# Performance work log

Measured on AMD Instinct MI355X. Metric: run time of the kernel, lower is better.

The kernel has to match this reference:

```python
import jax, jax.numpy as jnp
import numpy as np

B, NH, T, H, W = 2, 4, 8, 14, 14
DIM = 384
HD = DIM // NH  # 96 = head_dim = depthwise conv channels
N = T * H * W  # 1568 tokens, no cls
EPS = 1e-6


def _dwconv3d(x, w):
    # x: [BN, C, T, H, W], w: [C, 1, 3, 3, 3]; depthwise conv, stride 1, pad 1
    return jax.lax.conv_general_dilated(
        x, w, window_strides=(1, 1, 1), padding=[(1, 1)] * 3,
        feature_group_count=x.shape[1],
        dimension_numbers=('NCDHW', 'OIDHW', 'NCDHW'))


def _layernorm(x, g, b):
    m = jnp.mean(x, axis=-1, keepdims=True)
    v = jnp.var(x, axis=-1, keepdims=True)
    return (x - m) * jax.lax.rsqrt(v + EPS) * g + b


def _attention_pool(x4, conv_w, ln_g, ln_b, t, h, w):
    # x4: [B, nh, L, c] with L = t*h*w (no cls token)
    Bq, n, L, c = x4.shape
    y = x4.reshape(Bq * n, t, h, w, c).transpose(0, 4, 1, 2, 3)  # [(b nh), c, t, h, w]
    y = _dwconv3d(y, conv_w)
    y = y.transpose(0, 2, 3, 4, 1).reshape(Bq, n, L, c)
    return _layernorm(y, ln_g, ln_b)


def setup_inputs() -> dict:
    key = jax.random.key(0)
    ks = jax.random.split(key, 12)
    inp = {
        'x': jax.random.normal(ks[0], (B, N, DIM), jnp.float32),
        'qkv_w': jax.random.normal(ks[1], (3 * DIM, DIM), jnp.float32) * 0.02,
        'proj_w': jax.random.normal(ks[2], (DIM, DIM), jnp.float32) * 0.02,
        'proj_b': jnp.zeros((DIM,), jnp.float32),
        'pool_q_w': jax.random.normal(ks[3], (HD, 1, 3, 3, 3), jnp.float32) * 0.1,
        'pool_k_w': jax.random.normal(ks[4], (HD, 1, 3, 3, 3), jnp.float32) * 0.1,
        'pool_v_w': jax.random.normal(ks[5], (HD, 1, 3, 3, 3), jnp.float32) * 0.1,
        'norm_q_w': jnp.ones((HD,), jnp.float32), 'norm_q_b': jnp.zeros((HD,), jnp.float32),
        'norm_k_w': jnp.ones((HD,), jnp.float32), 'norm_k_b': jnp.zeros((HD,), jnp.float32),
        'norm_v_w': jnp.ones((HD,), jnp.float32), 'norm_v_b': jnp.zeros((HD,), jnp.float32),
        'rel_pos_h': jax.random.normal(ks[6], (2 * H - 1, HD), jnp.float32) * 0.02,
        'rel_pos_w': jax.random.normal(ks[7], (2 * W - 1, HD), jnp.float32) * 0.02,
        'rel_pos_t': jax.random.normal(ks[8], (2 * T - 1, HD), jnp.float32) * 0.02,
        't': T, 'h': H, 'w': W,
    }
    return inp


def reference(x, qkv_w, proj_w, proj_b, pool_q_w, pool_k_w, pool_v_w,
              norm_q_w, norm_q_b, norm_k_w, norm_k_b, norm_v_w, norm_v_b,
              rel_pos_h, rel_pos_w, rel_pos_t, t, h, w):
    Bq, Nq, _ = x.shape
    # fused QKV projection (qkv_bias=False)
    qkv = (x @ qkv_w.T).reshape(Bq, Nq, 3, NH, HD).transpose(2, 0, 3, 1, 4)
    q, k, v = qkv[0], qkv[1], qkv[2]  # [B, nh, N, hd]
    # pooled Q/K/V: depthwise conv3d + LayerNorm (stride 1 -> shapes preserved)
    q = _attention_pool(q, pool_q_w, norm_q_w, norm_q_b, t, h, w)
    k = _attention_pool(k, pool_k_w, norm_k_w, norm_k_b, t, h, w)
    v = _attention_pool(v, pool_v_w, norm_v_w, norm_v_b, t, h, w)

    scale = HD ** -0.5
    attn = jnp.einsum('bnqc,bnkc->bnqk', q * scale, k)  # [B, nh, N, N]

    # decomposed relative position biases (q_shape == k_shape, ratios == 1)
    dist_h = jnp.arange(h)[:, None] - jnp.arange(h)[None, :] + (h - 1)
    dist_w = jnp.arange(w)[:, None] - jnp.arange(w)[None, :] + (w - 1)
    dist_t = jnp.arange(t)[:, None] - jnp.arange(t)[None, :] + (t - 1)
    Rh = rel_pos_h[dist_h]  # [h, h, c]
    Rw = rel_pos_w[dist_w]  # [w, w, c]
    Rt = rel_pos_t[dist_t]  # [t, t, c]

    r_q = q.reshape(Bq, NH, t, h, w, HD)
    rel_h = jnp.einsum('bnthwc,hkc->bnthwk', r_q, Rh)  # [B,nh,t,h,w,kh]
    rel_w = jnp.einsum('bnthwc,wkc->bnthwk', r_q, Rw)  # [B,nh,t,h,w,kw]
    rel_t = jnp.einsum('bnthwc,tkc->bnthwk', r_q, Rt)  # [B,nh,t,h,w,kt]

    attn8 = attn.reshape(Bq, NH, t, h, w, t, h, w)
    attn8 = (attn8
             + rel_h[:, :, :, :, :, None, :, None]
             + rel_w[:, :, :, :, :, None, None, :]
             + rel_t[:, :, :, :, :, :, None, None])
    attn = jax.nn.softmax(attn8.reshape(Bq, NH, Nq, Nq), axis=-1)

    out = jnp.einsum('bnqk,bnkc->bnqc', attn, v)
    out = out + q  # residual pooling
    out = out.transpose(0, 2, 1, 3).reshape(Bq, Nq, DIM)
    out = out @ proj_w.T + proj_b
    return out
```

## Files before the change

kernel.cpp:

```cpp
#include <hip/hip_runtime.h>

#define B_    2
#define NH_   4
#define T_    8
#define H_    14
#define W_    14
#define HW_   196
#define HD_   96
#define DIM_  384
#define N_    1568
#define BH_   (B_*NH_)
#define BN_   (B_*N_)
#define BHN_  (BH_*N_)
#define CAUG_ 160

typedef unsigned short bf_t;
typedef unsigned int   u32;
typedef __attribute__((ext_vector_type(8))) short bf16x8;
typedef __attribute__((ext_vector_type(4))) float f32x4;

#define LOG2E 1.4426950408889634f
#define QSCALE_LOG2E 0.14724445f

static __device__ __forceinline__ float lo16(u32 v){ union{u32 i; float f;}x; x.i = v<<16;           return x.f; }
static __device__ __forceinline__ float hi16(u32 v){ union{u32 i; float f;}x; x.i = v & 0xffff0000u; return x.f; }
static __device__ __forceinline__ float b2f(bf_t v){ union{u32 i; float f;}x; x.i = ((u32)v)<<16;    return x.f; }
static __device__ __forceinline__ bf_t  f2b(float f){
  union{float f; u32 i;} x; x.f = f;
  return (bf_t)((x.i + 0x7fffu + ((x.i>>16)&1u)) >> 16);
}
static __device__ __forceinline__ u32 pack2(float a, float b){
  return (u32)f2b(a) | ((u32)f2b(b) << 16);
}

#define NA_ (BN_*DIM_)
#define NB_ (3*DIM_*DIM_)
#define NC_ (DIM_*DIM_)
#define CAST_BLOCKS ((NA_+NB_+NC_)/4/256)

__global__ __launch_bounds__(256) void k_cast(
    const float* __restrict__ a, bf_t* __restrict__ ad,
    const float* __restrict__ b, bf_t* __restrict__ bd,
    const float* __restrict__ c, bf_t* __restrict__ cd,
    const float* __restrict__ wq, const float* __restrict__ wk,
    const float* __restrict__ wv, float* __restrict__ tq,
    float* __restrict__ tk, float* __restrict__ tv){
  if (blockIdx.x < CAST_BLOCKS){
    const int i = blockIdx.x*256 + threadIdx.x;
    const int i4 = i*4;
    const float4* src; bf_t* dst; int off;
    if (i4 < NA_)           { src = (const float4*)a; dst = ad; off = i; }
    else if (i4 < NA_+NB_)  { src = (const float4*)b; dst = bd; off = i - NA_/4; }
    else                    { src = (const float4*)c; dst = cd; off = i - (NA_+NB_)/4; }
    const float4 v = src[off];
    ushort4 o; o.x = f2b(v.x); o.y = f2b(v.y); o.z = f2b(v.z); o.w = f2b(v.w);
    ((ushort4*)dst)[off] = o;
  } else {
    const int idx = (blockIdx.x - CAST_BLOCKS)*256 + threadIdx.x;
    if (idx >= 3*HD_*27) return;
    const int t = idx / (HD_*27), rem = idx % (HD_*27);
    const int ch = rem / 27, j = rem % 27;
    const float* s = (t==0)? wq : (t==1)? wk : wv;
    float* d       = (t==0)? tq : (t==1)? tk : tv;
    d[j*HD_ + ch] = s[ch*27 + j];
  }
}

__global__ __launch_bounds__(256) void k_qkv(const bf_t* __restrict__ Xb,
    const bf_t* __restrict__ Wb,
    bf_t* __restrict__ q, bf_t* __restrict__ k, bf_t* __restrict__ v){
  const int wid = threadIdx.x >> 6, lane = threadIdx.x & 63;
  const int wr = wid & 1, wc = wid >> 1;
  const int nl = lane & 15, quad = lane >> 4;
  const int r0 = blockIdx.x*64 + wr*32;
  const int c0 = blockIdx.y*128 + wc*64;
  f32x4 acc[2][4];
  #pragma unroll
  for (int i = 0; i < 2; ++i)
    #pragma unroll
    for (int j = 0; j < 4; ++j) acc[i][j] = (f32x4){0.f,0.f,0.f,0.f};
  const bf_t* A0 = Xb + (size_t)(r0 + nl)*DIM_ + quad*8;
  const bf_t* B0 = Wb + (size_t)(c0 + nl)*DIM_ + quad*8;
  #pragma unroll 2
  for (int k0 = 0; k0 < 12; ++k0){
    const bf16x8 a0 = *(const bf16x8*)(A0 + k0*32);
    const bf16x8 a1 = *(const bf16x8*)(A0 + 16*DIM_ + k0*32);
    bf16x8 bf[4];
    #pragma unroll
    for (int j = 0; j < 4; ++j) bf[j] = *(const bf16x8*)(B0 + (size_t)j*16*DIM_ + k0*32);
    #pragma unroll
    for (int j = 0; j < 4; ++j){
      acc[0][j] = __builtin_amdgcn_mfma_f32_16x16x32_bf16(a0, bf[j], acc[0][j], 0, 0, 0);
      acc[1][j] = __builtin_amdgcn_mfma_f32_16x16x32_bf16(a1, bf[j], acc[1][j], 0, 0, 0);
    }
  }
  #pragma unroll
  for (int i = 0; i < 2; ++i){
    #pragma unroll
    for (int r = 0; r < 4; ++r){
      const int m  = r0 + i*16 + quad*4 + r;
      const int bb = m / N_, nn = m % N_;
      #pragma unroll
      for (int j = 0; j < 4; ++j){
        const int col = c0 + j*16 + nl;
        const int s = col / DIM_, rem = col - s*DIM_;
        const int head = rem / HD_, hc = rem % HD_;
        bf_t* dst = (s==0) ? q : (s==1) ? k : v;
        dst[((size_t)(bb*NH_ + head)*N_ + nn)*HD_ + hc] = f2b(acc[i][j][r]);
      }
    }
  }
}

static __device__ __forceinline__ void conv_core(
    const bf_t* __restrict__ base, const float2* __restrict__ wgt,
    int n, int c0, float& v0, float& v1){
  const int tt = n / HW_; const int rm = n % HW_;
  const int hh = rm / W_, ww = rm % W_;
  u32 data[27];
  #pragma unroll
  for (int j = 0; j < 27; ++j){
    const int dt = j/9 - 1, dh = (j%9)/3 - 1, dw = j%3 - 1;
    const int t2 = tt+dt, h2 = hh+dh, w2 = ww+dw;
    const bool ok = ((unsigned)t2 < (unsigned)T_) && ((unsigned)h2 < (unsigned)H_)
                 && ((unsigned)w2 < (unsigned)W_);
    const int nn = ok ? (t2*HW_ + h2*W_ + w2) : n;
    const u32 d = *(const u32*)(base + (size_t)nn*HD_ + c0);
    data[j] = ok ? d : 0u;
  }
  v0 = 0.f; v1 = 0.f;
  #pragma unroll
  for (int j = 0; j < 27; ++j){
    v0 = fmaf(wgt[j].x, lo16(data[j]), v0);
    v1 = fmaf(wgt[j].y, hi16(data[j]), v1);
  }
}

static __device__ __forceinline__ void ln_butterfly(
    float v0, float v1, float& mean, float& rstd){
  float s  = v0 + v1;
  float s2 = v0*v0 + v1*v1;
  #pragma unroll
  for (int off = 32; off > 0; off >>= 1){
    s  += __shfl_xor(s,  off);
    s2 += __shfl_xor(s2, off);
  }
  mean = s * (1.f/HD_);
  const float var = fmaxf(s2*(1.f/HD_) - mean*mean, 0.f);
  rstd = rsqrtf(var + 1e-6f);
}

__global__ __launch_bounds__(256) void k_pool_all(
    const bf_t* __restrict__ qr_, const bf_t* __restrict__ kr_, const bf_t* __restrict__ vr_,
    const float* __restrict__ wtq, const float* __restrict__ wtk, const float* __restrict__ wtv,
    const float* __restrict__ gq, const float* __restrict__ bq,
    const float* __restrict__ gk, const float* __restrict__ bk,
    const float* __restrict__ gv, const float* __restrict__ bv,
    const float* __restrict__ rph, const float* __restrict__ rpw,
    const float* __restrict__ rpt,
    bf_t* __restrict__ qp, bf_t* __restrict__ Qaug,
    bf_t* __restrict__ Kt, bf_t* __restrict__ Vtt){
  __shared__ float qs[4][HD_];
  const int wid = threadIdx.x >> 6, lane = threadIdx.x & 63;
  const int bix = blockIdx.x;

  if (bix < BHN_/4){
    const int token = bix*4 + wid;
    const int bh = token / N_, n = token % N_;
    const int c0 = (lane < 48) ? 2*lane : 0;
    float2 wgt[27];
    #pragma unroll
    for (int j = 0; j < 27; ++j) wgt[j] = *(const float2*)(wtq + j*HD_ + c0);
    float v0, v1;
    conv_core(qr_ + (size_t)bh*N_*HD_, wgt, n, c0, v0, v1);
    if (lane >= 48){ v0 = 0.f; v1 = 0.f; }
    float mean, rstd;
    ln_butterfly(v0, v1, mean, rstd);
    if (lane < 48){
      const float y0 = (v0 - mean)*rstd*gq[c0]   + bq[c0];
      const float y1 = (v1 - mean)*rstd*gq[c0+1] + bq[c0+1];
      ((u32*)qp)  [(size_t)token*48 + lane] = pack2(y0, y1);
      ((u32*)Qaug)[(size_t)token*80 + lane] = pack2(y0*QSCALE_LOG2E, y1*QSCALE_LOG2E);
      qs[wid][c0] = y0; qs[wid][c0+1] = y1;
    }
    __syncthreads();
    const int tt = n / HW_; const int rm = n % HW_;
    const int hh = rm / W_, ww = rm % W_;
    if (lane < 36){
      const float* tb; int idx;
      if (lane < 14)      { tb = rph; idx = hh - lane      + 13; }
      else if (lane < 28) { tb = rpw; idx = ww - (lane-14) + 13; }
      else                { tb = rpt; idx = tt - (lane-28) +  7; }
      const float4* t4 = (const float4*)(tb + (size_t)idx*HD_);
      float acc = 0.f;
      #pragma unroll
      for (int i = 0; i < 24; ++i){
        const float4 rv = t4[i];
        acc += qs[wid][4*i]*rv.x + qs[wid][4*i+1]*rv.y
             + qs[wid][4*i+2]*rv.z + qs[wid][4*i+3]*rv.w;
      }
      Qaug[(size_t)token*CAUG_ + HD_ + lane] = f2b(acc * LOG2E);
    } else {
      Qaug[(size_t)token*CAUG_ + HD_ + lane] = 0;
    }
  } else if (bix < BHN_/2){
    const int token = (bix - BHN_/4)*4 + wid;
    const int bh = token / N_, n = token % N_;
    const int c0 = (lane < 48) ? 2*lane : 0;
    float2 wgt[27];
    #pragma unroll
    for (int j = 0; j < 27; ++j) wgt[j] = *(const float2*)(wtk + j*HD_ + c0);
    float v0, v1;
    conv_core(kr_ + (size_t)bh*N_*HD_, wgt, n, c0, v0, v1);
    if (lane >= 48){ v0 = 0.f; v1 = 0.f; }
    float mean, rstd;
    ln_butterfly(v0, v1, mean, rstd);
    const int tl = n >> 4, nr = n & 15;
    if (lane < 48){
      const float y0 = (v0 - mean)*rstd*gk[c0]   + bk[c0];
      const float y1 = (v1 - mean)*rstd*gk[c0+1] + bk[c0+1];
      const size_t idx = ((((size_t)bh*98 + tl)*5 + (lane>>4))*64
                         + ((lane&15)>>2)*16 + nr)*4 + (lane&3);
      ((u32*)Kt)[idx] = pack2(y0, y1);
    } else {
      const int tt = n / HW_; const int rm = n % HW_;
      const int hh = rm / W_, ww = rm % W_;
      const int m = lane - 48;
      u32 p[2];
      #pragma unroll
      for (int h2 = 0; h2 < 2; ++h2){
        u32 w_ = 0;
        #pragma unroll
        for (int e = 0; e < 2; ++e){
          const int jj = 4*m + 2*h2 + e;
          bool on = (jj < 14) ? (jj == hh) : (jj < 28) ? (jj-14 == ww)
                   : (jj < 36) ? (jj-28 == tt) : false;
          if (on) w_ |= (0x3F80u << (16*e));
        }
        p[h2] = w_;
      }
      const size_t base = ((((size_t)bh*98 + tl)*5 + (3 + (m>>3)))*64
                          + ((m&7)>>1)*16 + nr)*4 + 2*(m&1);
      *(uint2*)((u32*)Kt + base) = make_uint2(p[0], p[1]);
    }
  } else {
    const int tok0 = ((bix - BHN_/2)*4 + wid)*8;
    const int bh = tok0 / N_, n0 = tok0 % N_;
    const bf_t* base = vr_ + (size_t)bh*N_*HD_;
    const int c0 = (lane < 48) ? 2*lane : 0;
    float2 wgt[27];
    #pragma unroll
    for (int j = 0; j < 27; ++j) wgt[j] = *(const float2*)(wtv + j*HD_ + c0);
    const float gg0 = gv[c0], gg1 = gv[c0+1], bb0 = bv[c0], bb1 = bv[c0+1];
    u32 acc[8];
    #pragma unroll 1
    for (int t8 = 0; t8 < 8; ++t8){
      float v0, v1;
      conv_core(base, wgt, n0 + t8, c0, v0, v1);
      if (lane >= 48){ v0 = 0.f; v1 = 0.f; }
      float mean, rstd;
      ln_butterfly(v0, v1, mean, rstd);
      acc[t8] = pack2((v0 - mean)*rstd*gg0 + bb0, (v1 - mean)*rstd*gg1 + bb1);
    }
    if (lane < 48){
      u32 lo[4], hi[4];
      #pragma unroll
      for (int i = 0; i < 4; ++i){
        lo[i] = (acc[2*i] & 0xffffu)  | (acc[2*i+1] << 16);
        hi[i] = (acc[2*i] >> 16)      | (acc[2*i+1] & 0xffff0000u);
      }
      const int pr = n0 >> 5, qd = (n0 & 31) >> 3;
      const int ct0 = lane >> 3, nl0 = 2*(lane & 7);
      bf_t* g0 = Vtt + ((((size_t)bh*49 + pr)*6 + ct0)*64 + qd*16 + nl0)*8;
      *(uint4*)g0       = make_uint4(lo[0], lo[1], lo[2], lo[3]);
      *(uint4*)(g0 + 8) = make_uint4(hi[0], hi[1], hi[2], hi[3]);
    }
  }
}

__global__ __launch_bounds__(512) void k_attn(
    const bf_t* __restrict__ Qaug, const bf_t* __restrict__ Kt,
    const bf_t* __restrict__ Vtt, const bf_t* __restrict__ qp,
    bf_t* __restrict__ attb){
  __shared__ __align__(16) short Pb[8][16][40];
  __shared__ float Os[8][16][96];
  __shared__ float ms[8][16], ls[8][16];
  const int wid = threadIdx.x >> 6, lane = threadIdx.x & 63;
  const int bh = blockIdx.x / 98, qt = blockIdx.x % 98;
  const int q0 = qt*16;
  const int nl = lane & 15, quad = lane >> 4;

  bf16x8 qa[5];
  {
    const bf_t* Qrow = Qaug + ((size_t)bh*N_ + q0 + nl)*CAUG_ + quad*8;
    #pragma unroll
    for (int i = 0; i < 5; ++i) qa[i] = *(const bf16x8*)(Qrow + i*32);
  }
  short* Pw = &Pb[wid][0][0];

  f32x4 O[6];
  #pragma unroll
  for (int i = 0; i < 6; ++i) O[i] = (f32x4){0.f,0.f,0.f,0.f};
  float mc[4]   = {0.f,0.f,0.f,0.f};
  float rmax[4] = {-3e38f,-3e38f,-3e38f,-3e38f};
  float l[4]    = {0.f,0.f,0.f,0.f};

  auto s_tile = [&](int tl, int half){
    const bf_t* Kp = Kt + (((size_t)bh*98 + tl)*5*64 + lane)*8;
    f32x4 s = (f32x4){0.f,0.f,0.f,0.f};
    #pragma unroll
    for (int i = 0; i < 5; ++i)
      s = __builtin_amdgcn_mfma_f32_16x16x32_bf16(qa[i], *(const bf16x8*)(Kp + i*512), s, 0, 0, 0);
    #pragma unroll
    for (int r = 0; r < 4; ++r){
      rmax[r] = fmaxf(rmax[r], s[r]);
      const float p = exp2f(s[r] - mc[r]);
      l[r] += p;
      Pw[(quad*4 + r)*40 + half*16 + nl] = (short)f2b(p);
    }
  };
  auto rescale = [&](){
    #pragma unroll
    for (int r = 0; r < 4; ++r){
      float tm = rmax[r];
      tm = fmaxf(tm, __shfl_xor(tm, 1));
      tm = fmaxf(tm, __shfl_xor(tm, 2));
      tm = fmaxf(tm, __shfl_xor(tm, 4));
      tm = fmaxf(tm, __shfl_xor(tm, 8));
      const float mn = fmaxf(mc[r], tm);
      const float al = exp2f(mc[r] - mn);
      mc[r] = mn; l[r] *= al;
      #pragma unroll
      for (int ct = 0; ct < 6; ++ct) O[ct][r] *= al;
    }
  };

  const int p0 = (wid == 0) ? 0 : (7 + 6*(wid-1));
  const int npairs = (wid == 0) ? 7 : 6;
  #pragma unroll 1
  for (int pi = 0; pi < npairs; ++pi){
    const int kp = p0 + pi;
    s_tile(2*kp,     0);
    s_tile(2*kp + 1, 1);
    const bf16x8 pa = *(const bf16x8*)(Pw + nl*40 + quad*8);
    const bf_t* Vp = Vtt + (((size_t)bh*49 + kp)*6*64 + lane)*8;
    #pragma unroll
    for (int ct = 0; ct < 6; ++ct)
      O[ct] = __builtin_amdgcn_mfma_f32_16x16x32_bf16(pa, *(const bf16x8*)(Vp + ct*512), O[ct], 0, 0, 0);
    if (pi == npairs-1) rescale();
  }

  #pragma unroll
  for (int r = 0; r < 4; ++r){
    float ls_ = l[r];
    ls_ += __shfl_xor(ls_, 1); ls_ += __shfl_xor(ls_, 2);
    ls_ += __shfl_xor(ls_, 4); ls_ += __shfl_xor(ls_, 8);
    if (nl == 0){ ms[wid][quad*4 + r] = mc[r]; ls[wid][quad*4 + r] = ls_; }
    #pragma unroll
    for (int ct = 0; ct < 6; ++ct) Os[wid][quad*4 + r][ct*16 + nl] = O[ct][r];
  }
  __syncthreads();

  const int bb = bh >> 2, head = bh & 3;
  for (int e = threadIdx.x; e < 16*96; e += 512){
    const int row = e / 96, col = e % 96;
    float mx = -3e38f;
    #pragma unroll
    for (int w = 0; w < 8; ++w) mx = fmaxf(mx, ms[w][row]);
    float L = 0.f, A = 0.f;
    #pragma unroll
    for (int w = 0; w < 8; ++w){
      const float wt = exp2f(ms[w][row] - mx);
      L += wt*ls[w][row];
      A += wt*Os[w][row][col];
    }
    const int qg = q0 + row;
    const float val = A/L + b2f(qp[((size_t)bh*N_ + qg)*HD_ + col]);
    attb[((size_t)(bb*N_ + qg))*DIM_ + head*HD_ + col] = f2b(val);
  }
}

__global__ __launch_bounds__(256) void k_proj(const bf_t* __restrict__ Ab,
    const bf_t* __restrict__ Wpb, const float* __restrict__ pb,
    float* __restrict__ out){
  const int wid = threadIdx.x >> 6, lane = threadIdx.x & 63;
  const int wr = wid & 1, wc = wid >> 1;
  const int nl = lane & 15, quad = lane >> 4;
  const int r0 = blockIdx.x*64 + wr*32;
  const int c0 = blockIdx.y*128 + wc*64;
  f32x4 acc[2][4];
  #pragma unroll
  for (int i = 0; i < 2; ++i)
    #pragma unroll
    for (int j = 0; j < 4; ++j) acc[i][j] = (f32x4){0.f,0.f,0.f,0.f};
  const bf_t* A0 = Ab  + (size_t)(r0 + nl)*DIM_ + quad*8;
  const bf_t* B0 = Wpb + (size_t)(c0 + nl)*DIM_ + quad*8;
  #pragma unroll 2
  for (int k0 = 0; k0 < 12; ++k0){
    const bf16x8 a0 = *(const bf16x8*)(A0 + k0*32);
    const bf16x8 a1 = *(const bf16x8*)(A0 + 16*DIM_ + k0*32);
    bf16x8 bf[4];
    #pragma unroll
    for (int j = 0; j < 4; ++j) bf[j] = *(const bf16x8*)(B0 + (size_t)j*16*DIM_ + k0*32);
    #pragma unroll
    for (int j = 0; j < 4; ++j){
      acc[0][j] = __builtin_amdgcn_mfma_f32_16x16x32_bf16(a0, bf[j], acc[0][j], 0, 0, 0);
      acc[1][j] = __builtin_amdgcn_mfma_f32_16x16x32_bf16(a1, bf[j], acc[1][j], 0, 0, 0);
    }
  }
  #pragma unroll
  for (int i = 0; i < 2; ++i){
    #pragma unroll
    for (int r = 0; r < 4; ++r){
      const int m = r0 + i*16 + quad*4 + r;
      #pragma unroll
      for (int j = 0; j < 4; ++j){
        const int col = c0 + j*16 + nl;
        out[(size_t)m*DIM_ + col] = acc[i][j][r] + pb[col];
      }
    }
  }
}

extern "C" void kernel_launch(void* const* d_in, const int* in_sizes, int n_in,
                              void* d_out, int out_size, void* d_ws, size_t ws_size,
                              hipStream_t stream){
  const float* x      = (const float*)d_in[0];
  const float* qkv_w  = (const float*)d_in[1];
  const float* proj_w = (const float*)d_in[2];
  const float* proj_b = (const float*)d_in[3];
  const float* pqw    = (const float*)d_in[4];
  const float* pkw    = (const float*)d_in[5];
  const float* pvw    = (const float*)d_in[6];
  const float* nqw    = (const float*)d_in[7];
  const float* nqb    = (const float*)d_in[8];
  const float* nkw    = (const float*)d_in[9];
  const float* nkb    = (const float*)d_in[10];
  const float* nvw    = (const float*)d_in[11];
  const float* nvb    = (const float*)d_in[12];
  const float* rph    = (const float*)d_in[13];
  const float* rpw    = (const float*)d_in[14];
  const float* rpt    = (const float*)d_in[15];

  char* p = (char*)d_ws;
  const size_t RAW = (size_t)BH_*N_*HD_*2;
  const size_t AUG = (size_t)BH_*N_*CAUG_*2;
  bf_t* xb     = (bf_t*)(p);
  bf_t* wqkvb  = (bf_t*)(p + RAW);
  bf_t* wprojb = (bf_t*)(p + RAW + 884736);
  char* p2 = p + RAW + 884736 + 294912;
  bf_t* raw_q  = (bf_t*)(p2);
  bf_t* raw_k  = (bf_t*)(p2 + RAW);
  bf_t* raw_v  = (bf_t*)(p2 + 2*RAW);
  bf_t* attb   = raw_q;
  bf_t* qp     = (bf_t*)(p2 + 3*RAW);
  bf_t* Qaug   = (bf_t*)(p2 + 4*RAW);
  bf_t* Kt     = (bf_t*)(p2 + 4*RAW + AUG);
  bf_t* Vtt    = (bf_t*)(p2 + 4*RAW + 2*AUG);
  float* wtq   = (float*)(p2 + 4*RAW + 2*AUG + RAW);
  float* wtk   = wtq + 27*HD_;
  float* wtv   = wtk + 27*HD_;

  k_cast    <<<CAST_BLOCKS + 31,  256, 0, stream>>>(x, xb, qkv_w, wqkvb, proj_w, wprojb,
                                                    pqw, pkw, pvw, wtq, wtk, wtv);
  k_qkv     <<<dim3(BN_/64, 9),   256, 0, stream>>>(xb, wqkvb, raw_q, raw_k, raw_v);
  k_pool_all<<<BHN_/2 + BHN_/32,  256, 0, stream>>>(raw_q, raw_k, raw_v,
                                                    wtq, wtk, wtv,
                                                    nqw, nqb, nkw, nkb, nvw, nvb,
                                                    rph, rpw, rpt,
                                                    qp, Qaug, Kt, Vtt);
  k_attn    <<<BH_*98,            512, 0, stream>>>(Qaug, Kt, Vtt, qp, attb);
  k_proj    <<<dim3(BN_/64, 3),   256, 0, stream>>>(attb, wprojb, proj_b, (float*)d_out);
}
```

Baseline: 234.5 us.

## Stage conv halo slab in shared memory for pooled q/k/v depthwise conv

Replaces the per-token global gathers of the 3x3x3 depthwise conv with a block-wide shared-memory slab of 90 neighbouring rows covering 8 consecutive tokens. Each block now handles 8 tokens of one of q/k/v, with a uniform grid of 3*1568 blocks. The goal is to cut redundant global/L2 reads of neighbours, at the cost of loading 90 rows per 8 tokens and extra barriers. The V transpose now goes through shared memory.

```diff
diff --git a/kernel.cpp b/kernel.cpp
--- a/kernel.cpp
+++ b/kernel.cpp
@@ -112,30 +112,6 @@
   }
 }
 
-static __device__ __forceinline__ void conv_core(
-    const bf_t* __restrict__ base, const float2* __restrict__ wgt,
-    int n, int c0, float& v0, float& v1){
-  const int tt = n / HW_; const int rm = n % HW_;
-  const int hh = rm / W_, ww = rm % W_;
-  u32 data[27];
-  #pragma unroll
-  for (int j = 0; j < 27; ++j){
-    const int dt = j/9 - 1, dh = (j%9)/3 - 1, dw = j%3 - 1;
-    const int t2 = tt+dt, h2 = hh+dh, w2 = ww+dw;
-    const bool ok = ((unsigned)t2 < (unsigned)T_) && ((unsigned)h2 < (unsigned)H_)
-                 && ((unsigned)w2 < (unsigned)W_);
-    const int nn = ok ? (t2*HW_ + h2*W_ + w2) : n;
-    const u32 d = *(const u32*)(base + (size_t)nn*HD_ + c0);
-    data[j] = ok ? d : 0u;
-  }
-  v0 = 0.f; v1 = 0.f;
-  #pragma unroll
-  for (int j = 0; j < 27; ++j){
-    v0 = fmaf(wgt[j].x, lo16(data[j]), v0);
-    v1 = fmaf(wgt[j].y, hi16(data[j]), v1);
-  }
-}
-
 static __device__ __forceinline__ void ln_butterfly(
     float v0, float v1, float& mean, float& rstd){
   float s  = v0 + v1;
@@ -150,7 +126,7 @@
   rstd = rsqrtf(var + 1e-6f);
 }
 
-__global__ __launch_bounds__(256) void k_pool_all(
+__global__ __launch_bounds__(256) void k_pool_slab(
     const bf_t* __restrict__ qr_, const bf_t* __restrict__ kr_, const bf_t* __restrict__ vr_,
     const float* __restrict__ wtq, const float* __restrict__ wtk, const float* __restrict__ wtv,
     const float* __restrict__ gq, const float* __restrict__ bq,
@@ -160,120 +136,129 @@
     const float* __restrict__ rpt,
     bf_t* __restrict__ qp, bf_t* __restrict__ Qaug,
     bf_t* __restrict__ Kt, bf_t* __restrict__ Vtt){
-  __shared__ float qs[4][HD_];
+  __shared__ __align__(16) bf_t slab[90][HD_];
+  __shared__ float qtmp[4][2][HD_];
+  __shared__ u32 vres[8][48];
   const int wid = threadIdx.x >> 6, lane = threadIdx.x & 63;
-  const int bix = blockIdx.x;
-
-  if (bix < BHN_/4){
-    const int token = bix*4 + wid;
-    const int bh = token / N_, n = token % N_;
-    const int c0 = (lane < 48) ? 2*lane : 0;
-    float2 wgt[27];
-    #pragma unroll
-    for (int j = 0; j < 27; ++j) wgt[j] = *(const float2*)(wtq + j*HD_ + c0);
-    float v0, v1;
-    conv_core(qr_ + (size_t)bh*N_*HD_, wgt, n, c0, v0, v1);
+  const int sec = blockIdx.x / 1568;
+  const int rr_ = blockIdx.x % 1568;
+  const int bh = rr_ / 196, tok0 = (rr_ % 196)*8;
+  const bf_t*  src = (sec==0)? qr_ : (sec==1)? kr_ : vr_;
+  const float* wt  = (sec==0)? wtq : (sec==1)? wtk : wtv;
+  const float* g   = (sec==0)? gq  : (sec==1)? gk  : gv;
+  const float* be  = (sec==0)? bq  : (sec==1)? bk  : bv;
+  const bf_t* base = src + (size_t)bh*N_*HD_;
+
+  for (int li = threadIdx.x; li < 90*12; li += 256){
+    const int rw = li / 12, ss = li % 12;
+    const int dt = rw/30 - 1, dh = (rw%30)/10 - 1, dwp = rw%10 - 1;
+    int nn = tok0 + dt*HW_ + dh*W_ + dwp;
+    nn = min(max(nn, 0), N_-1);
+    *(uint4*)&slab[rw][ss*8] = *(const uint4*)(base + (size_t)nn*HD_ + ss*8);
+  }
+  __syncthreads();
+
+  const int c0 = (lane < 48) ? 2*lane : 0;
+  float2 wgt[27];
+  #pragma unroll
+  for (int j = 0; j < 27; ++j) wgt[j] = *(const float2*)(wt + j*HD_ + c0);
+  const float gg0 = g[c0], gg1 = g[c0+1], be0 = be[c0], be1 = be[c0+1];
+
+  #pragma unroll
+  for (int tk = 0; tk < 2; ++tk){
+    const int u = wid*2 + tk;
+    const int n = tok0 + u;
+    const int tt = n / HW_; const int rm = n % HW_;
+    const int hh = rm / W_, ww = rm % W_;
+    float v0 = 0.f, v1 = 0.f;
+    #pragma unroll
+    for (int j = 0; j < 27; ++j){
+      const int dt = j/9 - 1, dh = (j%9)/3 - 1, dw = j%3 - 1;
+      const bool ok = ((unsigned)(tt+dt) < (unsigned)T_)
+                   && ((unsigned)(hh+dh) < (unsigned)H_)
+                   && ((unsigned)(ww+dw) < (unsigned)W_);
+      const int rj = (dt+1)*30 + (dh+1)*10 + (dw + u + 1);
+      u32 d = *(const u32*)&slab[rj][c0];
+      d = ok ? d : 0u;
+      v0 = fmaf(wgt[j].x, lo16(d), v0);
+      v1 = fmaf(wgt[j].y, hi16(d), v1);
+    }
     if (lane >= 48){ v0 = 0.f; v1 = 0.f; }
     float mean, rstd;
     ln_butterfly(v0, v1, mean, rstd);
-    if (lane < 48){
-      const float y0 = (v0 - mean)*rstd*gq[c0]   + bq[c0];
-      const float y1 = (v1 - mean)*rstd*gq[c0+1] + bq[c0+1];
-      ((u32*)qp)  [(size_t)token*48 + lane] = pack2(y0, y1);
-      ((u32*)Qaug)[(size_t)token*80 + lane] = pack2(y0*QSCALE_LOG2E, y1*QSCALE_LOG2E);
-      qs[wid][c0] = y0; qs[wid][c0+1] = y1;
-    }
+    const float y0 = (v0 - mean)*rstd*gg0 + be0;
+    const float y1 = (v1 - mean)*rstd*gg1 + be1;
+
+    if (sec == 0){
+      const int token = bh*N_ + n;
+      if (lane < 48){
+        ((u32*)qp)  [(size_t)token*48 + lane] = pack2(y0, y1);
+        ((u32*)Qaug)[(size_t)token*80 + lane] = pack2(y0*QSCALE_LOG2E, y1*QSCALE_LOG2E);
+        qtmp[wid][tk][c0] = y0; qtmp[wid][tk][c0+1] = y1;
+      }
+      __syncthreads();
+      if (lane < 36){
+        const float* tb; int idx;
+        if (lane < 14)      { tb = rph; idx = hh - lane      + 13; }
+        else if (lane < 28) { tb = rpw; idx = ww - (lane-14) + 13; }
+        else                { tb = rpt; idx = tt - (lane-28) +  7; }
+        const float4* t4 = (const float4*)(tb + (size_t)idx*HD_);
+        float acc = 0.f;
+        #pragma unroll
+        for (int i = 0; i < 24; ++i){
+          const float4 rv = t4[i];
+          acc += qtmp[wid][tk][4*i]*rv.x + qtmp[wid][tk][4*i+1]*rv.y
+               + qtmp[wid][tk][4*i+2]*rv.z + qtmp[wid][tk][4*i+3]*rv.w;
+        }
+        Qaug[(size_t)token*CAUG_ + HD_ + lane] = f2b(acc * LOG2E);
+      } else if (lane < 64){
+        Qaug[(size_t)token*CAUG_ + HD_ + lane] = 0;
+      }
+    } else if (sec == 1){
+      const int tl = n >> 4, nr = n & 15;
+      if (lane < 48){
+        const size_t idx = ((((size_t)bh*98 + tl)*5 + (lane>>4))*64
+                           + ((lane&15)>>2)*16 + nr)*4 + (lane&3);
+        ((u32*)Kt)[idx] = pack2(y0, y1);
+      } else {
+        const int m = lane - 48;
+        u32 pr_[2];
+        #pragma unroll
+        for (int h2 = 0; h2 < 2; ++h2){
+          u32 w_ = 0;
+          #pragma unroll
+          for (int e = 0; e < 2; ++e){
+            const int jj = 4*m + 2*h2 + e;
+            bool on = (jj < 14) ? (jj == hh) : (jj < 28) ? (jj-14 == ww)
+                     : (jj < 36) ? (jj-28 == tt) : false;
+            if (on) w_ |= (0x3F80u << (16*e));
+          }
+          pr_[h2] = w_;
+        }
+        const size_t bidx = ((((size_t)bh*98 + tl)*5 + (3 + (m>>3)))*64
+                            + ((m&7)>>1)*16 + nr)*4 + 2*(m&1);
+        *(uint2*)((u32*)Kt + bidx) = make_uint2(pr_[0], pr_[1]);
+      }
+    } else {
+      if (lane < 48) vres[u][lane] = pack2(y0, y1);
+    }
+  }
+
+  if (sec == 2){
     __syncthreads();
-    const int tt = n / HW_; const int rm = n % HW_;
-    const int hh = rm / W_, ww = rm % W_;
-    if (lane < 36){
-      const float* tb; int idx;
-      if (lane < 14)      { tb = rph; idx = hh - lane      + 13; }
-      else if (lane < 28) { tb = rpw; idx = ww - (lane-14) + 13; }
-      else                { tb = rpt; idx = tt - (lane-28) +  7; }
-      const float4* t4 = (const float4*)(tb + (size_t)idx*HD_);
-      float acc = 0.f;
-      #pragma unroll
-      for (int i = 0; i < 24; ++i){
-        const float4 rv = t4[i];
-        acc += qs[wid][4*i]*rv.x + qs[wid][4*i+1]*rv.y
-             + qs[wid][4*i+2]*rv.z + qs[wid][4*i+3]*rv.w;
-      }
-      Qaug[(size_t)token*CAUG_ + HD_ + lane] = f2b(acc * LOG2E);
-    } else {
-      Qaug[(size_t)token*CAUG_ + HD_ + lane] = 0;
-    }
-  } else if (bix < BHN_/2){
-    const int token = (bix - BHN_/4)*4 + wid;
-    const int bh = token / N_, n = token % N_;
-    const int c0 = (lane < 48) ? 2*lane : 0;
-    float2 wgt[27];
-    #pragma unroll
-    for (int j = 0; j < 27; ++j) wgt[j] = *(const float2*)(wtk + j*HD_ + c0);
-    float v0, v1;
-    conv_core(kr_ + (size_t)bh*N_*HD_, wgt, n, c0, v0, v1);
-    if (lane >= 48){ v0 = 0.f; v1 = 0.f; }
-    float mean, rstd;
-    ln_butterfly(v0, v1, mean, rstd);
-    const int tl = n >> 4, nr = n & 15;
-    if (lane < 48){
-      const float y0 = (v0 - mean)*rstd*gk[c0]   + bk[c0];
-      const float y1 = (v1 - mean)*rstd*gk[c0+1] + bk[c0+1];
-      const size_t idx = ((((size_t)bh*98 + tl)*5 + (lane>>4))*64
-                         + ((lane&15)>>2)*16 + nr)*4 + (lane&3);
-      ((u32*)Kt)[idx] = pack2(y0, y1);
-    } else {
-      const int tt = n / HW_; const int rm = n % HW_;
-      const int hh = rm / W_, ww = rm % W_;
-      const int m = lane - 48;
-      u32 p[2];
-      #pragma unroll
-      for (int h2 = 0; h2 < 2; ++h2){
-        u32 w_ = 0;
-        #pragma unroll
-        for (int e = 0; e < 2; ++e){
-          const int jj = 4*m + 2*h2 + e;
-          bool on = (jj < 14) ? (jj == hh) : (jj < 28) ? (jj-14 == ww)
-                   : (jj < 36) ? (jj-28 == tt) : false;
-          if (on) w_ |= (0x3F80u << (16*e));
-        }
-        p[h2] = w_;
-      }
-      const size_t base = ((((size_t)bh*98 + tl)*5 + (3 + (m>>3)))*64
-                          + ((m&7)>>1)*16 + nr)*4 + 2*(m&1);
-      *(uint2*)((u32*)Kt + base) = make_uint2(p[0], p[1]);
-    }
-  } else {
-    const int tok0 = ((bix - BHN_/2)*4 + wid)*8;
-    const int bh = tok0 / N_, n0 = tok0 % N_;
-    const bf_t* base = vr_ + (size_t)bh*N_*HD_;
-    const int c0 = (lane < 48) ? 2*lane : 0;
-    float2 wgt[27];
-    #pragma unroll
-    for (int j = 0; j < 27; ++j) wgt[j] = *(const float2*)(wtv + j*HD_ + c0);
-    const float gg0 = gv[c0], gg1 = gv[c0+1], bb0 = bv[c0], bb1 = bv[c0+1];
-    u32 acc[8];
-    #pragma unroll 1
-    for (int t8 = 0; t8 < 8; ++t8){
-      float v0, v1;
-      conv_core(base, wgt, n0 + t8, c0, v0, v1);
-      if (lane >= 48){ v0 = 0.f; v1 = 0.f; }
-      float mean, rstd;
-      ln_butterfly(v0, v1, mean, rstd);
-      acc[t8] = pack2((v0 - mean)*rstd*gg0 + bb0, (v1 - mean)*rstd*gg1 + bb1);
-    }
-    if (lane < 48){
-      u32 lo[4], hi[4];
+    if (threadIdx.x < HD_){
+      const int c = threadIdx.x;
+      u32 o[4];
       #pragma unroll
       for (int i = 0; i < 4; ++i){
-        lo[i] = (acc[2*i] & 0xffffu)  | (acc[2*i+1] << 16);
-        hi[i] = (acc[2*i] >> 16)      | (acc[2*i+1] & 0xffff0000u);
-      }
-      const int pr = n0 >> 5, qd = (n0 & 31) >> 3;
-      const int ct0 = lane >> 3, nl0 = 2*(lane & 7);
-      bf_t* g0 = Vtt + ((((size_t)bh*49 + pr)*6 + ct0)*64 + qd*16 + nl0)*8;
-      *(uint4*)g0       = make_uint4(lo[0], lo[1], lo[2], lo[3]);
-      *(uint4*)(g0 + 8) = make_uint4(hi[0], hi[1], hi[2], hi[3]);
+        const u32 a = vres[2*i][c>>1], b = vres[2*i+1][c>>1];
+        const u32 ra = (c&1) ? (a >> 16) : (a & 0xffffu);
+        const u32 rb = (c&1) ? (b >> 16) : (b & 0xffffu);
+        o[i] = ra | (rb << 16);
+      }
+      const int pr = tok0 >> 5, qd = (tok0 & 31) >> 3;
+      bf_t* dst = Vtt + ((((size_t)bh*49 + pr)*6 + (c>>4))*64 + qd*16 + (c&15))*8;
+      *(uint4*)dst = make_uint4(o[0], o[1], o[2], o[3]);
     }
   }
 }
@@ -461,14 +446,14 @@
   float* wtk   = wtq + 27*HD_;
   float* wtv   = wtk + 27*HD_;
 
-  k_cast    <<<CAST_BLOCKS + 31,  256, 0, stream>>>(x, xb, qkv_w, wqkvb, proj_w, wprojb,
+  k_cast     <<<CAST_BLOCKS + 31, 256, 0, stream>>>(x, xb, qkv_w, wqkvb, proj_w, wprojb,
                                                     pqw, pkw, pvw, wtq, wtk, wtv);
-  k_qkv     <<<dim3(BN_/64, 9),   256, 0, stream>>>(xb, wqkvb, raw_q, raw_k, raw_v);
-  k_pool_all<<<BHN_/2 + BHN_/32,  256, 0, stream>>>(raw_q, raw_k, raw_v,
+  k_qkv      <<<dim3(BN_/64, 9),  256, 0, stream>>>(xb, wqkvb, raw_q, raw_k, raw_v);
+  k_pool_slab<<<3*1568,           256, 0, stream>>>(raw_q, raw_k, raw_v,
                                                     wtq, wtk, wtv,
                                                     nqw, nqb, nkw, nkb, nvw, nvb,
                                                     rph, rpw, rpt,
                                                     qp, Qaug, Kt, Vtt);
-  k_attn    <<<BH_*98,            512, 0, stream>>>(Qaug, Kt, Vtt, qp, attb);
-  k_proj    <<<dim3(BN_/64, 3),   256, 0, stream>>>(attb, wprojb, proj_b, (float*)d_out);
-}
+  k_attn     <<<BH_*98,           512, 0, stream>>>(Qaug, Kt, Vtt, qp, attb);
+  k_proj     <<<dim3(BN_/64, 3),  256, 0, stream>>>(attb, wprojb, proj_b, (float*)d_out);
+}
```

Result: faster. 221.1 us (-5.7%).
